# Kernel tuning notes

Hardware: AMD Instinct MI355X
Metric: run time of the kernel (lower is better)

Reference implementation:

```python
import jax, jax.numpy as jnp
import numpy as np

B, Q, K, DQ, DK, DV, H = 16, 64, 512, 512, 512, 512, 256
MASK_VAL = -1e6


def setup_inputs() -> dict:
    key = jax.random.key(0)
    k1, k2, k3, k4, k5, k6, k7 = jax.random.split(key, 7)
    return {
        "queries": jax.random.normal(k1, (B, Q, DQ), dtype=jnp.float32),
        "keys": jax.random.normal(k2, (B, K, DK), dtype=jnp.float32),
        "values": jax.random.normal(k3, (B, K, DV), dtype=jnp.float32),
        "valid_lens": jax.random.randint(k4, (B,), 1, K + 1, dtype=jnp.int32),
        "Wq": jax.random.normal(k5, (DQ, H), dtype=jnp.float32) * (1.0 / np.sqrt(DQ)),
        "Wk": jax.random.normal(k6, (DK, H), dtype=jnp.float32) * (1.0 / np.sqrt(DK)),
        "Wv": jax.random.normal(k7, (H,), dtype=jnp.float32) * (1.0 / np.sqrt(H)),
    }


def reference(queries, keys, values, valid_lens, Wq, Wk, Wv):
    # Project queries and keys into the shared additive-attention space.
    q = jnp.einsum("bqd,dh->bqh", queries, Wq)   # [B,Q,H]
    k = jnp.einsum("bkd,dh->bkh", keys, Wk)      # [B,K,H]
    # Bahdanau additive scoring: tanh(q + k) projected to a scalar per (q,k).
    feats = jnp.tanh(q[:, :, None, :] + k[:, None, :, :])  # [B,Q,K,H]
    scores = jnp.einsum("bqkh,h->bqk", feats, Wv)           # [B,Q,K]
    # Masked softmax over the key axis (positions >= valid_len masked out).
    mask = jnp.arange(K)[None, None, :] < valid_lens[:, None, None]  # [B,1,K]
    scores = jnp.where(mask, scores, MASK_VAL)
    attn = jax.nn.softmax(scores, axis=-1)                  # [B,Q,K]
    # Dropout is identity in eval mode; weighted sum of values.
    return jnp.einsum("bqk,bkv->bqv", attn, values)         # [B,Q,DV]
```

## Files before the change

kernel.cpp:

```cpp
#include <hip/hip_runtime.h>

#define LOG2E 1.4426950408889634f
#define TWO_LOG2E 2.8853900817779268f

typedef __attribute__((ext_vector_type(8))) short short8;
typedef __attribute__((ext_vector_type(4))) float f32x4;

__device__ __forceinline__ float e2x(float v) {
    return __builtin_amdgcn_exp2f(v * TWO_LOG2E);
}

__device__ __forceinline__ void split2(float x, float y, unsigned& hi, unsigned& lo) {
    unsigned ux = __float_as_uint(x), uy = __float_as_uint(y);
    float hx = __uint_as_float(ux & 0xffff0000u);
    float hy = __uint_as_float(uy & 0xffff0000u);
    unsigned lx = __float_as_uint(x - hx), ly = __float_as_uint(y - hy);
    hi = (ux >> 16) | (uy & 0xffff0000u);
    lo = (lx >> 16) | (ly & 0xffff0000u);
}

__global__ __launch_bounds__(256) void wprep_kernel(const float* __restrict__ Wq,
                                                    const float* __restrict__ Wk,
                                                    ushort* __restrict__ Wq2T,
                                                    ushort* __restrict__ Wk2T) {
    __shared__ float T[64][65];
    const float* W  = blockIdx.z ? Wk : Wq;
    ushort* W2T     = blockIdx.z ? Wk2T : Wq2T;
    const int t  = threadIdx.x;
    const int k0 = blockIdx.x * 64;
    const int n0 = blockIdx.y * 64;
#pragma unroll
    for (int p = 0; p < 4; ++p) {
        int u  = t + p * 256;
        int kk = u >> 4;
        int nf = (u & 15) * 4;
        float4 w = *reinterpret_cast<const float4*>(&W[(size_t)(k0 + kk) * 256 + n0 + nf]);
        T[nf + 0][kk] = w.x; T[nf + 1][kk] = w.y;
        T[nf + 2][kk] = w.z; T[nf + 3][kk] = w.w;
    }
    __syncthreads();
#pragma unroll
    for (int p = 0; p < 4; ++p) {
        int u  = t + p * 256;
        int n  = u >> 4;
        int kf = (u & 15) * 4;
        float a = T[n][kf], b = T[n][kf + 1], c = T[n][kf + 2], d = T[n][kf + 3];
        unsigned h01, l01, h23, l23;
        split2(a, b, h01, l01);
        split2(c, d, h23, l23);
        int kg   = k0 + kf;
        int ng   = n0 + n;
        int tile = ng >> 6;
        int row  = ng & 63;
        int cc   = kg >> 5;
        int kpos = kg & 31;
        ushort* base = W2T + (size_t)(tile * 16 + cc) * 6144
                     + (kpos >> 3) * 512 + row * 8 + (kpos & 7);
        uint2 hi; hi.x = h01; hi.y = h23;
        uint2 lo; lo.x = l01; lo.y = l23;
        *reinterpret_cast<uint2*>(base)        = hi;
        *reinterpret_cast<uint2*>(base + 2048) = hi;
        *reinterpret_cast<uint2*>(base + 4096) = lo;
    }
}

__global__ __launch_bounds__(256) void mfma_proj_kernel(const float* __restrict__ queries,
                                                        const float* __restrict__ keys,
                                                        const ushort* __restrict__ Wq2T,
                                                        const ushort* __restrict__ Wk2T,
                                                        float* __restrict__ Eq,
                                                        float* __restrict__ Ekp) {
    __shared__ float smemf[4736];
    ushort* Ah = reinterpret_cast<ushort*>(smemf);
    ushort* Bl = reinterpret_cast<ushort*>(smemf) + 3328;

    const int t    = threadIdx.x;
    const int mt   = blockIdx.x;
    const int Nb   = blockIdx.y * 64;
    const bool isQ = mt < 32;
    const int mloc = (isQ ? mt : mt - 32) * 32;
    const float4* Asrc4 = reinterpret_cast<const float4*>(isQ ? queries : keys)
                        + (size_t)mloc * 128;
    const ushort* W2T = isQ ? Wq2T : Wk2T;

    const int ln15 = t & 15;
    const int q    = (t >> 4) & 3;
    const int w    = t >> 6;
    const int wn   = w * 16;
    const int am   = t >> 3;
    const int ak   = t & 7;

    const char* gB[3];
#pragma unroll
    for (int i = 0; i < 3; ++i)
        gB[i] = reinterpret_cast<const char*>(W2T) + (size_t)(Nb >> 6) * 196608
              + i * 4096 + t * 16;

    f32x4 acc[2];
    acc[0] = (f32x4)0.0f;
    acc[1] = (f32x4)0.0f;

    float4 ra = Asrc4[(size_t)am * 128 + ak];

    for (int c = 0; c < 16; ++c) {
        __syncthreads();
#pragma unroll
        for (int i = 0; i < 3; ++i) {
            __builtin_amdgcn_global_load_lds(
                reinterpret_cast<const unsigned int*>(gB[i]),
                reinterpret_cast<unsigned int*>(
                    reinterpret_cast<char*>(smemf) + 6656 + i * 4096 + (t >> 6) * 1024),
                16, 0, 0);
            gB[i] += 12288;
        }
        {
            unsigned h01, l01, h23, l23;
            split2(ra.x, ra.y, h01, l01);
            split2(ra.z, ra.w, h23, l23);
            uint2 hi; hi.x = h01; hi.y = h23;
            uint2 lo; lo.x = l01; lo.y = l23;
            ushort* row = Ah + am * 104 + ak * 4;
            *reinterpret_cast<uint2*>(row)      = hi;
            *reinterpret_cast<uint2*>(row + 32) = lo;
            *reinterpret_cast<uint2*>(row + 64) = hi;
        }
        if (c < 15) ra = Asrc4[(size_t)am * 128 + (c + 1) * 8 + ak];
        __syncthreads();
#pragma unroll
        for (int s = 0; s < 3; ++s) {
            short8 af[2], bf;
#pragma unroll
            for (int fm = 0; fm < 2; ++fm)
                af[fm] = *reinterpret_cast<const short8*>(
                    Ah + (fm * 16 + ln15) * 104 + s * 32 + q * 8);
            bf = *reinterpret_cast<const short8*>(
                Bl + (s * 4 + q) * 512 + (wn + ln15) * 8);
#pragma unroll
            for (int fm = 0; fm < 2; ++fm)
                acc[fm] = __builtin_amdgcn_mfma_f32_16x16x32_bf16(
                    af[fm], bf, acc[fm], 0, 0, 0);
        }
    }

    if (isQ) {
#pragma unroll
        for (int fm = 0; fm < 2; ++fm)
#pragma unroll
            for (int r = 0; r < 4; ++r) {
                int row = mloc + fm * 16 + q * 4 + r;
                int col = Nb + wn + ln15;
                Eq[(size_t)row * 256 + col] = e2x(acc[fm][r]);
            }
    } else {
        __syncthreads();
        float (*Cs)[33] = reinterpret_cast<float(*)[33]>(smemf);
#pragma unroll
        for (int fm = 0; fm < 2; ++fm)
#pragma unroll
            for (int r = 0; r < 4; ++r) {
                int m_l = fm * 16 + q * 4 + r;
                int n_l = wn + ln15;
                Cs[n_l][m_l] = acc[fm][r];
            }
        __syncthreads();
        const int b      = mloc >> 9;
        const int k0h    = (mloc & 511) >> 1;
        const int h2base = Nb >> 1;
        float4* out4 = reinterpret_cast<float4*>(Ekp);
#pragma unroll
        for (int p = 0; p < 2; ++p) {
            int u   = t + p * 256;
            int h2r = u >> 4;
            int kp  = u & 15;
            int kk  = kp * 2;
            float4 o;
            o.x = e2x(Cs[2 * h2r    ][kk    ]);
            o.y = e2x(Cs[2 * h2r + 1][kk    ]);
            o.z = e2x(Cs[2 * h2r    ][kk + 1]);
            o.w = e2x(Cs[2 * h2r + 1][kk + 1]);
            out4[(size_t)b * 32768 + (size_t)(h2base + h2r) * 256 + k0h + kp] = o;
        }
    }
}

__global__ __launch_bounds__(256) void attn_kernel(
        const float* __restrict__ Eq, const float* __restrict__ Ekp,
        const float* __restrict__ Wv, const int* __restrict__ valid_lens,
        const float* __restrict__ values, float* __restrict__ out) {
    __shared__ __align__(16) float Eqs[4][256];
    __shared__ float Wvs[256];
    __shared__ __align__(16) float P[4][512];
    __shared__ float Sd[4][4];

    const int t  = threadIdx.x;
    const int q0 = blockIdx.x * 4;
    const int b  = blockIdx.y;

    const float4* eq4 = reinterpret_cast<const float4*>(Eq + (size_t)(b * 64 + q0) * 256);
    *reinterpret_cast<float4*>(&Eqs[t >> 6][(t & 63) * 4]) = eq4[t];
    Wvs[t] = Wv[t];
    __syncthreads();

    const float2* ekp2 = reinterpret_cast<const float2*>(Ekp) + (size_t)b * 65536 + t;
    float accA[4] = {0.f, 0.f, 0.f, 0.f};
    float accB[4] = {0.f, 0.f, 0.f, 0.f};
#pragma unroll 4
    for (int h2 = 0; h2 < 128; ++h2) {
        float2 ekA = ekp2[h2 * 512];
        float2 ekB = ekp2[h2 * 512 + 256];
        float2 wv  = *reinterpret_cast<const float2*>(&Wvs[2 * h2]);
#pragma unroll
        for (int q = 0; q < 4; ++q) {
            float2 e = *reinterpret_cast<const float2*>(&Eqs[q][2 * h2]);
            float a0 = fmaf(e.x, ekA.x, 1.0f);
            float a1 = fmaf(e.y, ekA.y, 1.0f);
            accA[q] = fmaf(fmaf(wv.y, a0, wv.x * a1),
                           __builtin_amdgcn_rcpf(a0 * a1), accA[q]);
            float b0 = fmaf(e.x, ekB.x, 1.0f);
            float b1 = fmaf(e.y, ekB.y, 1.0f);
            accB[q] = fmaf(fmaf(wv.y, b0, wv.x * b1),
                           __builtin_amdgcn_rcpf(b0 * b1), accB[q]);
        }
    }

    const int vl = valid_lens[b];
    float EA[4], EB[4], part[4];
#pragma unroll
    for (int q = 0; q < 4; ++q) {
        float sA = -2.0f * accA[q];
        float sB = -2.0f * accB[q];
        EA[q] = (t       < vl) ? __builtin_amdgcn_exp2f(sA * LOG2E) : 0.0f;
        EB[q] = (t + 256 < vl) ? __builtin_amdgcn_exp2f(sB * LOG2E) : 0.0f;
        part[q] = EA[q] + EB[q];
    }
#pragma unroll
    for (int off = 32; off > 0; off >>= 1)
#pragma unroll
        for (int q = 0; q < 4; ++q) part[q] += __shfl_xor(part[q], off);
    if ((t & 63) == 0) {
#pragma unroll
        for (int q = 0; q < 4; ++q) Sd[t >> 6][q] = part[q];
    }
    __syncthreads();
#pragma unroll
    for (int q = 0; q < 4; ++q) {
        float inv = 1.0f / ((Sd[0][q] + Sd[1][q]) + (Sd[2][q] + Sd[3][q]));
        P[q][t]       = EA[q] * inv;
        P[q][t + 256] = EB[q] * inv;
    }
    __syncthreads();

    const float2* V2 = reinterpret_cast<const float2*>(values) + (size_t)b * 131072 + t;
    float2 av[4];
#pragma unroll
    for (int q = 0; q < 4; ++q) av[q] = make_float2(0.f, 0.f);

#pragma unroll 4
    for (int k4 = 0; k4 < 128; ++k4) {
        float2 v0 = V2[(size_t)(k4 * 4 + 0) * 256];
        float2 v1 = V2[(size_t)(k4 * 4 + 1) * 256];
        float2 v2 = V2[(size_t)(k4 * 4 + 2) * 256];
        float2 v3 = V2[(size_t)(k4 * 4 + 3) * 256];
#pragma unroll
        for (int q = 0; q < 4; ++q) {
            float4 p = *reinterpret_cast<const float4*>(&P[q][k4 * 4]);
            av[q].x = fmaf(p.x, v0.x, av[q].x); av[q].y = fmaf(p.x, v0.y, av[q].y);
            av[q].x = fmaf(p.y, v1.x, av[q].x); av[q].y = fmaf(p.y, v1.y, av[q].y);
            av[q].x = fmaf(p.z, v2.x, av[q].x); av[q].y = fmaf(p.z, v2.y, av[q].y);
            av[q].x = fmaf(p.w, v3.x, av[q].x); av[q].y = fmaf(p.w, v3.y, av[q].y);
        }
    }

    float* ob = out + (size_t)(b * 64 + q0) * 512 + 2 * t;
#pragma unroll
    for (int q = 0; q < 4; ++q)
        *reinterpret_cast<float2*>(ob + (size_t)q * 512) = av[q];
}

extern "C" void kernel_launch(void* const* d_in, const int* in_sizes, int n_in,
                              void* d_out, int out_size, void* d_ws, size_t ws_size,
                              hipStream_t stream) {
    (void)in_sizes; (void)n_in; (void)out_size; (void)ws_size;
    const float* queries    = (const float*)d_in[0];
    const float* keys       = (const float*)d_in[1];
    const float* values     = (const float*)d_in[2];
    const int*   valid_lens = (const int*)d_in[3];
    const float* Wq         = (const float*)d_in[4];
    const float* Wk         = (const float*)d_in[5];
    const float* Wv         = (const float*)d_in[6];
    float* out = (float*)d_out;

    float* ws     = (float*)d_ws;
    float* Eq     = ws;
    float* Ekp    = ws + 262144;
    ushort* Wq2T  = (ushort*)(ws + 2883584);
    ushort* Wk2T  = Wq2T + 393216;

    hipLaunchKernelGGL(wprep_kernel, dim3(8, 4, 2), dim3(256), 0, stream,
                       Wq, Wk, Wq2T, Wk2T);
    hipLaunchKernelGGL(mfma_proj_kernel, dim3(288, 4), dim3(256), 0, stream,
                       queries, keys, Wq2T, Wk2T, Eq, Ekp);
    hipLaunchKernelGGL(attn_kernel, dim3(16, 16), dim3(256), 0, stream,
                       Eq, Ekp, Wv, valid_lens, values, out);
}
```

Baseline: 153.5 us.

## Double attention block threads to one key per thread and remap block-to-batch order

The attention kernel now runs 512 threads per block, so each thread scores a single key instead of two. The value-weighted sum is split across two key halves, and the partial sums are combined through shared memory before the store. The 1D grid is also remapped so consecutive blocks cover different batches, which may change how L2 and HBM accesses are spread. The aim is more in-flight wavefronts and shorter per-thread dependency chains, at the cost of an extra barrier and a reduction step.

```diff
diff --git a/kernel.cpp b/kernel.cpp
--- a/kernel.cpp
+++ b/kernel.cpp
@@ -183,55 +183,53 @@
     }
 }
 
-__global__ __launch_bounds__(256) void attn_kernel(
+__global__ __launch_bounds__(512) void attn_kernel(
         const float* __restrict__ Eq, const float* __restrict__ Ekp,
         const float* __restrict__ Wv, const int* __restrict__ valid_lens,
         const float* __restrict__ values, float* __restrict__ out) {
     __shared__ __align__(16) float Eqs[4][256];
     __shared__ float Wvs[256];
     __shared__ __align__(16) float P[4][512];
-    __shared__ float Sd[4][4];
-
-    const int t  = threadIdx.x;
-    const int q0 = blockIdx.x * 4;
-    const int b  = blockIdx.y;
-
-    const float4* eq4 = reinterpret_cast<const float4*>(Eq + (size_t)(b * 64 + q0) * 256);
-    *reinterpret_cast<float4*>(&Eqs[t >> 6][(t & 63) * 4]) = eq4[t];
-    Wvs[t] = Wv[t];
+    __shared__ float Sd[8][4];
+    __shared__ __align__(16) float2 Pc[4][256];
+
+    const int t   = threadIdx.x;
+    const int lid = blockIdx.x;
+    const int r  = lid & 7;
+    const int j  = lid >> 3;
+    const int b  = r + 8 * (j & 1);
+    const int q0 = (j >> 1) * 4;
+
+    if (t < 256) {
+        const float4* eq4 = reinterpret_cast<const float4*>(Eq + (size_t)(b * 64 + q0) * 256);
+        *reinterpret_cast<float4*>(&Eqs[t >> 6][(t & 63) * 4]) = eq4[t];
+        Wvs[t] = Wv[t];
+    }
     __syncthreads();
 
     const float2* ekp2 = reinterpret_cast<const float2*>(Ekp) + (size_t)b * 65536 + t;
-    float accA[4] = {0.f, 0.f, 0.f, 0.f};
-    float accB[4] = {0.f, 0.f, 0.f, 0.f};
-#pragma unroll 4
+    float acc[4] = {0.f, 0.f, 0.f, 0.f};
+#pragma unroll 8
     for (int h2 = 0; h2 < 128; ++h2) {
-        float2 ekA = ekp2[h2 * 512];
-        float2 ekB = ekp2[h2 * 512 + 256];
-        float2 wv  = *reinterpret_cast<const float2*>(&Wvs[2 * h2]);
+        float2 ek = ekp2[h2 * 512];
+        float2 wv = *reinterpret_cast<const float2*>(&Wvs[2 * h2]);
 #pragma unroll
         for (int q = 0; q < 4; ++q) {
             float2 e = *reinterpret_cast<const float2*>(&Eqs[q][2 * h2]);
-            float a0 = fmaf(e.x, ekA.x, 1.0f);
-            float a1 = fmaf(e.y, ekA.y, 1.0f);
-            accA[q] = fmaf(fmaf(wv.y, a0, wv.x * a1),
-                           __builtin_amdgcn_rcpf(a0 * a1), accA[q]);
-            float b0 = fmaf(e.x, ekB.x, 1.0f);
-            float b1 = fmaf(e.y, ekB.y, 1.0f);
-            accB[q] = fmaf(fmaf(wv.y, b0, wv.x * b1),
-                           __builtin_amdgcn_rcpf(b0 * b1), accB[q]);
+            float a0 = fmaf(e.x, ek.x, 1.0f);
+            float a1 = fmaf(e.y, ek.y, 1.0f);
+            acc[q] = fmaf(fmaf(wv.y, a0, wv.x * a1),
+                          __builtin_amdgcn_rcpf(a0 * a1), acc[q]);
         }
     }
 
     const int vl = valid_lens[b];
-    float EA[4], EB[4], part[4];
+    float E[4], part[4];
 #pragma unroll
     for (int q = 0; q < 4; ++q) {
-        float sA = -2.0f * accA[q];
-        float sB = -2.0f * accB[q];
-        EA[q] = (t       < vl) ? __builtin_amdgcn_exp2f(sA * LOG2E) : 0.0f;
-        EB[q] = (t + 256 < vl) ? __builtin_amdgcn_exp2f(sB * LOG2E) : 0.0f;
-        part[q] = EA[q] + EB[q];
+        float s = -2.0f * acc[q];
+        E[q] = (t < vl) ? __builtin_amdgcn_exp2f(s * LOG2E) : 0.0f;
+        part[q] = E[q];
     }
 #pragma unroll
     for (int off = 32; off > 0; off >>= 1)
@@ -244,26 +242,29 @@
     __syncthreads();
 #pragma unroll
     for (int q = 0; q < 4; ++q) {
-        float inv = 1.0f / ((Sd[0][q] + Sd[1][q]) + (Sd[2][q] + Sd[3][q]));
-        P[q][t]       = EA[q] * inv;
-        P[q][t + 256] = EB[q] * inv;
-    }
-    __syncthreads();
-
-    const float2* V2 = reinterpret_cast<const float2*>(values) + (size_t)b * 131072 + t;
+        float d = ((Sd[0][q] + Sd[1][q]) + (Sd[2][q] + Sd[3][q]))
+                + ((Sd[4][q] + Sd[5][q]) + (Sd[6][q] + Sd[7][q]));
+        P[q][t] = E[q] * (1.0f / d);
+    }
+    __syncthreads();
+
+    const int v2c = t & 255;
+    const int kh  = t >> 8;
+    const float2* V2 = reinterpret_cast<const float2*>(values)
+                     + (size_t)b * 131072 + (size_t)(kh * 256) * 256 + v2c;
     float2 av[4];
 #pragma unroll
     for (int q = 0; q < 4; ++q) av[q] = make_float2(0.f, 0.f);
 
 #pragma unroll 4
-    for (int k4 = 0; k4 < 128; ++k4) {
+    for (int k4 = 0; k4 < 64; ++k4) {
         float2 v0 = V2[(size_t)(k4 * 4 + 0) * 256];
         float2 v1 = V2[(size_t)(k4 * 4 + 1) * 256];
         float2 v2 = V2[(size_t)(k4 * 4 + 2) * 256];
         float2 v3 = V2[(size_t)(k4 * 4 + 3) * 256];
 #pragma unroll
         for (int q = 0; q < 4; ++q) {
-            float4 p = *reinterpret_cast<const float4*>(&P[q][k4 * 4]);
+            float4 p = *reinterpret_cast<const float4*>(&P[q][kh * 256 + k4 * 4]);
             av[q].x = fmaf(p.x, v0.x, av[q].x); av[q].y = fmaf(p.x, v0.y, av[q].y);
             av[q].x = fmaf(p.y, v1.x, av[q].x); av[q].y = fmaf(p.y, v1.y, av[q].y);
             av[q].x = fmaf(p.z, v2.x, av[q].x); av[q].y = fmaf(p.z, v2.y, av[q].y);
@@ -271,10 +272,20 @@
         }
     }
 
-    float* ob = out + (size_t)(b * 64 + q0) * 512 + 2 * t;
-#pragma unroll
-    for (int q = 0; q < 4; ++q)
-        *reinterpret_cast<float2*>(ob + (size_t)q * 512) = av[q];
+    if (kh == 1) {
+#pragma unroll
+        for (int q = 0; q < 4; ++q) Pc[q][v2c] = av[q];
+    }
+    __syncthreads();
+    if (kh == 0) {
+        float* ob = out + (size_t)(b * 64 + q0) * 512 + 2 * v2c;
+#pragma unroll
+        for (int q = 0; q < 4; ++q) {
+            float2 o = Pc[q][v2c];
+            o.x += av[q].x; o.y += av[q].y;
+            *reinterpret_cast<float2*>(ob + (size_t)q * 512) = o;
+        }
+    }
 }
 
 extern "C" void kernel_launch(void* const* d_in, const int* in_sizes, int n_in,
@@ -300,6 +311,6 @@
                        Wq, Wk, Wq2T, Wk2T);
     hipLaunchKernelGGL(mfma_proj_kernel, dim3(288, 4), dim3(256), 0, stream,
                        queries, keys, Wq2T, Wk2T, Eq, Ekp);
-    hipLaunchKernelGGL(attn_kernel, dim3(16, 16), dim3(256), 0, stream,
+    hipLaunchKernelGGL(attn_kernel, dim3(256), dim3(512), 0, stream,
                        Eq, Ekp, Wv, valid_lens, values, out);
 }
```

Measured after the change: 147.0 us. 4.2% less time.
